# Performance work log

Hardware: AMD Instinct MI355X
Metric: run time of the kernel (lower is better)

Reference implementation:

```python
import jax, jax.numpy as jnp
import numpy as np

B = 65536          # number of graphs
NPG = 28           # nodes per graph (896 = 32*28)
N = B * NPG
K = 4              # random within-graph neighbors per node


def setup_inputs() -> dict:
    key = jax.random.key(0)
    ks = jax.random.split(key, 8)
    x = jax.random.normal(ks[0], (N, 2), dtype=jnp.float32)
    # within-graph random edges: each node i -> K random targets in its graph
    local = jax.random.randint(ks[1], (N, K), 0, NPG)
    base = (jnp.arange(N, dtype=jnp.int32) // NPG) * NPG
    dst = (base[:, None] + local.astype(jnp.int32)).reshape(-1)
    src = jnp.repeat(jnp.arange(N, dtype=jnp.int32), K)
    edge_index = jnp.stack([src, dst])  # [2, E]
    conv_w = jax.random.normal(ks[2], (2, 32), dtype=jnp.float32) * (1.0 / np.sqrt(2))
    conv_b = jax.random.normal(ks[3], (32,), dtype=jnp.float32) * 0.01
    fc1_w = jax.random.normal(ks[4], (896, 256), dtype=jnp.float32) * (1.0 / np.sqrt(896))
    fc1_b = jax.random.normal(ks[5], (256,), dtype=jnp.float32) * 0.01
    fc2_w = jax.random.normal(ks[6], (256, 2), dtype=jnp.float32) * (1.0 / np.sqrt(256))
    fc2_b = jax.random.normal(ks[7], (2,), dtype=jnp.float32) * 0.01
    return {"x": x, "edge_index": edge_index, "conv_w": conv_w, "conv_b": conv_b,
            "fc1_w": fc1_w, "fc1_b": fc1_b, "fc2_w": fc2_w, "fc2_b": fc2_b}


def gcn_conv(x, edge_index, w, b):
    n = x.shape[0]
    h = x @ w  # [N, 32]
    loops = jnp.arange(n, dtype=edge_index.dtype)
    src = jnp.concatenate([edge_index[0], loops])
    dst = jnp.concatenate([edge_index[1], loops])
    deg = jax.ops.segment_sum(jnp.ones_like(dst, dtype=h.dtype), dst, num_segments=n)
    dinv = jnp.where(deg > 0, jax.lax.rsqrt(jnp.maximum(deg, 1.0)), 0.0)
    norm = dinv[src] * dinv[dst]  # [E']
    agg = jax.ops.segment_sum(h[src] * norm[:, None], dst, num_segments=n)
    return agg + b


def reference(x, edge_index, conv_w, conv_b, fc1_w, fc1_b, fc2_w, fc2_b):
    h = jax.nn.relu(gcn_conv(x, edge_index, conv_w, conv_b))  # [N, 32]
    h = h.reshape(-1, 896)                                    # [B, 896]
    h = h @ fc1_w + fc1_b                                     # [B, 256]
    nrm = jnp.sqrt(jnp.sum(h * h, axis=1, keepdims=True))
    hn = h / jnp.maximum(nrm, 1e-12)                          # F.normalize(dim=1)
    x1 = hn @ fc2_w + fc2_b                                   # [B, 2]
    mu = jax.nn.sigmoid(x1[:, 0])
    theta = jax.nn.softplus(x1[:, 1])
    return hn, mu, theta
```

## Files before the change

kernel.cpp:

```cpp
#include <hip/hip_runtime.h>
#include <hip/hip_bf16.h>
#include <stdint.h>

#define NPG 28
#define KDIM 896
#define NOUT 256
#define BM 64
#define BK 32
#define KT (KDIM / BK)

typedef __attribute__((ext_vector_type(8))) __bf16 bf16x8;
typedef __attribute__((ext_vector_type(8))) ushort us8;
typedef __attribute__((ext_vector_type(4))) float f32x4;

__device__ __forceinline__ ushort f2bf(float v) {
    uint u = __float_as_uint(v);
    return (ushort)((u + 0x7fffu + ((u >> 16) & 1u)) >> 16);
}

__device__ __forceinline__ void gload_lds16(const void* g, void* l) {
    __builtin_amdgcn_global_load_lds(
        (const __attribute__((address_space(1))) void*)(uintptr_t)g,
        (__attribute__((address_space(3))) void*)(uintptr_t)l,
        16, 0, 0);
}

__global__ __launch_bounds__(256) void k_agg(
    const float* __restrict__ x, const int* __restrict__ dst,
    const float* __restrict__ f1w,
    float* __restrict__ acc2g, ushort* __restrict__ wt, int nAgg)
{
    __shared__ int   pk[8][32];
    __shared__ float sx[8][32][2];
    __shared__ float t[32][33];

    const int tid = threadIdx.x;

    if ((int)blockIdx.x >= nAgg) {
        int b = blockIdx.x - nAgg;
        int n0 = (b & 7) * 32, k0 = (b >> 3) * 32;
        int tx = tid & 31, ty = tid >> 5;
#pragma unroll
        for (int q = 0; q < 4; ++q)
            t[ty + q * 8][tx] = f1w[(k0 + ty + q * 8) * NOUT + n0 + tx];
        __syncthreads();
#pragma unroll
        for (int q = 0; q < 4; ++q)
            wt[(long)(n0 + ty + q * 8) * KDIM + k0 + tx] = f2bf(t[tx][ty + q * 8]);
        return;
    }

    const int g = tid >> 5;
    const int j = tid & 31;
    const long gb = ((long)blockIdx.x * 8 + g) * NPG;

    float2 xx = make_float2(0.f, 0.f);
    if (j < NPG) {
        int4 d4 = ((const int4*)dst)[gb + j];
        xx = ((const float2*)x)[gb + j];
        int gbi = (int)gb;
        pk[g][j] = (d4.x - gbi) | ((d4.y - gbi) << 8) |
                   ((d4.z - gbi) << 16) | ((d4.w - gbi) << 24);
    }
    __syncthreads();

    const uint repj = (uint)j * 0x01010101u;
    uint cp0 = 0, cp1 = 0, cp2 = 0, cp3 = 0;
    int cnt = 0;
#pragma unroll
    for (int s4 = 0; s4 < 7; ++s4) {
        int4 pv = *(const int4*)&pk[g][s4 * 4];
#pragma unroll
        for (int r = 0; r < 4; ++r) {
            uint v = ((const uint*)&pv)[r] ^ repj;
            uint zb = ~(((v & 0x7F7F7F7Fu) + 0x7F7F7F7Fu) | v) & 0x80808080u;
            uint c = (uint)__popc(zb);
            cnt += (int)c;
            int s = s4 * 4 + r;
            uint nib = c << ((s & 7) * 4);
            if (s < 8)       cp0 |= nib;
            else if (s < 16) cp1 |= nib;
            else if (s < 24) cp2 |= nib;
            else             cp3 |= nib;
        }
    }

    const float dinv = rsqrtf((float)(1 + cnt));
    const float sx0 = xx.x * dinv, sx1 = xx.y * dinv;
    if (j < NPG) {
        sx[g][j][0] = sx0;
        sx[g][j][1] = sx1;
    }
    __syncthreads();

    float a0 = sx0, a1 = sx1;
#pragma unroll
    for (int s = 0; s < NPG; ++s) {
        float2 sv = *(const float2*)&sx[g][s][0];
        uint cpw = (s < 8) ? cp0 : (s < 16) ? cp1 : (s < 24) ? cp2 : cp3;
        float cf = (float)((cpw >> ((s & 7) * 4)) & 0xFu);
        a0 += cf * sv.x;
        a1 += cf * sv.y;
    }

    if (j < NPG) {
        const long Btot = (long)nAgg * 8;
        const long graph = (long)blockIdx.x * 8 + g;
        ((float2*)acc2g)[(long)j * Btot + graph] = make_float2(a0 * dinv, a1 * dinv);
    }
}

__device__ __forceinline__ void stage_b4(const char* WtB, ushort* BsX, int kt, int w, int l) {
    const int o = (l & 3) ^ ((l >> 3) & 3);
#pragma unroll
    for (int i = 0; i < 4; ++i) {
        int row = w * 64 + i * 16 + (l >> 2);
        gload_lds16(WtB + (long)row * (KDIM * 2) + kt * 64 + o * 16,
                    (char*)BsX + w * 4096 + i * 1024);
    }
}

__device__ __forceinline__ void agen_write(ushort* AsX, float2 av, int awoff,
                                           const float* w0, const float* w1, const float* bb) {
    union { us8 v; uint u[4]; } pk;
#pragma unroll
    for (int k = 0; k < 4; ++k) {
        float e0 = fmaxf(av.x * w0[2 * k]     + av.y * w1[2 * k]     + bb[2 * k],     0.f);
        float e1 = fmaxf(av.x * w0[2 * k + 1] + av.y * w1[2 * k + 1] + bb[2 * k + 1], 0.f);
        __hip_bfloat162 h = __float22bfloat162_rn(make_float2(e0, e1));
        pk.u[k] = *reinterpret_cast<uint*>(&h);
    }
    *(us8*)&AsX[awoff] = pk.v;
}

__device__ __forceinline__ void compute_mfma(const ushort* AsX, const ushort* BsX,
                                             f32x4 acc[4][4], int a_off, int b_off) {
    bf16x8 bfr[4], afr[4];
#pragma unroll
    for (int ni = 0; ni < 4; ++ni)
        bfr[ni] = *(const bf16x8*)(&BsX[b_off + ni * 512]);
#pragma unroll
    for (int mi = 0; mi < 4; ++mi)
        afr[mi] = *(const bf16x8*)(&AsX[a_off + mi * 512]);
    __builtin_amdgcn_s_setprio(1);
#pragma unroll
    for (int mi = 0; mi < 4; ++mi)
#pragma unroll
        for (int ni = 0; ni < 4; ++ni)
            acc[mi][ni] = __builtin_amdgcn_mfma_f32_16x16x32_bf16(
                afr[mi], bfr[ni], acc[mi][ni], 0, 0, 0);
    __builtin_amdgcn_s_setprio(0);
}

__global__ __launch_bounds__(256, 3) void k_gemm(
    const float* __restrict__ acc2g, const ushort* __restrict__ Wt,
    const float* __restrict__ cw, const float* __restrict__ cb,
    const float* __restrict__ f1b, const float* __restrict__ f2w,
    const float* __restrict__ f2b, float* __restrict__ out, int Bsz)
{
    __shared__ ushort As0[BM * BK], As1[BM * BK];
    __shared__ ushort Bs0[NOUT * BK], Bs1[NOUT * BK];

    const int tid = threadIdx.x;
    const int w = tid >> 6, l = tid & 63;
    const int l15 = l & 15, lhi = (l >> 4) & 3;
    const long m0 = (long)blockIdx.x * BM;
    const long Btot = Bsz;

    const int ao = __builtin_amdgcn_readfirstlane(w);
    const int awoff = l * 32 + ((ao ^ ((l >> 1) & 3)) * 8);
    float w0[8], w1[8], bb[8];
#pragma unroll
    for (int k = 0; k < 8; ++k) {
        w0[k] = cw[ao * 8 + k]; w1[k] = cw[32 + ao * 8 + k]; bb[k] = cb[ao * 8 + k];
    }

    const int swz = (lhi ^ ((l15 >> 1) & 3)) * 8;
    const int a_off = l15 * 32 + swz;
    const int b_off = (w * 64 + l15) * 32 + swz;

    const float2* a2 = (const float2*)acc2g;
    const char* WtB = (const char*)Wt;
    const long ag = m0 + l;

    f32x4 acc[4][4];
#pragma unroll
    for (int mi = 0; mi < 4; ++mi)
#pragma unroll
        for (int ni = 0; ni < 4; ++ni) acc[mi][ni] = (f32x4){0.f, 0.f, 0.f, 0.f};

    {
        float2 av0 = a2[ag];
        stage_b4(WtB, Bs0, 0, w, l);
        agen_write(As0, av0, awoff, w0, w1, bb);
    }
    float2 avn = a2[Btot + ag];
    __syncthreads();

    for (int kt = 0; kt < KT - 2; kt += 2) {
        stage_b4(WtB, Bs1, kt + 1, w, l);
        float2 avn2 = a2[(long)(kt + 2) * Btot + ag];
        agen_write(As1, avn, awoff, w0, w1, bb);
        compute_mfma(As0, Bs0, acc, a_off, b_off);
        asm volatile("s_waitcnt lgkmcnt(0)" ::: "memory");
        __builtin_amdgcn_s_barrier();
        asm volatile("s_waitcnt vmcnt(0)" ::: "memory");

        stage_b4(WtB, Bs0, kt + 2, w, l);
        avn = a2[(long)(kt + 3) * Btot + ag];
        agen_write(As0, avn2, awoff, w0, w1, bb);
        compute_mfma(As1, Bs1, acc, a_off, b_off);
        asm volatile("s_waitcnt lgkmcnt(0)" ::: "memory");
        __builtin_amdgcn_s_barrier();
        asm volatile("s_waitcnt vmcnt(0)" ::: "memory");
    }
    {
        stage_b4(WtB, Bs1, KT - 1, w, l);
        agen_write(As1, avn, awoff, w0, w1, bb);
        compute_mfma(As0, Bs0, acc, a_off, b_off);
        asm volatile("s_waitcnt lgkmcnt(0)" ::: "memory");
        __builtin_amdgcn_s_barrier();
        asm volatile("s_waitcnt vmcnt(0)" ::: "memory");
        compute_mfma(As1, Bs1, acc, a_off, b_off);
    }
    __syncthreads();

    float b1[4], w20[4], w21[4];
#pragma unroll
    for (int ni = 0; ni < 4; ++ni) {
        int col = w * 64 + ni * 16 + l15;
        b1[ni] = f1b[col];
        w20[ni] = f2w[col * 2 + 0];
        w21[ni] = f2w[col * 2 + 1];
    }
    float* red    = (float*)As0;
    float* red_ss = red;
    float* red_p0 = red + 256;
    float* red_p1 = red + 512;
    float* red_rn = red + 768;

#pragma unroll
    for (int mi = 0; mi < 4; ++mi) {
        float ssr[4], p0r[4], p1r[4];
#pragma unroll
        for (int r = 0; r < 4; ++r) { ssr[r] = 0.f; p0r[r] = 0.f; p1r[r] = 0.f; }
#pragma unroll
        for (int ni = 0; ni < 4; ++ni) {
#pragma unroll
            for (int r = 0; r < 4; ++r) {
                float v = acc[mi][ni][r] + b1[ni];
                acc[mi][ni][r] = v;
                ssr[r] += v * v;
                p0r[r] += v * w20[ni];
                p1r[r] += v * w21[ni];
            }
        }
#pragma unroll
        for (int m = 1; m < 16; m <<= 1) {
#pragma unroll
            for (int r = 0; r < 4; ++r) {
                ssr[r] += __shfl_xor(ssr[r], m);
                p0r[r] += __shfl_xor(p0r[r], m);
                p1r[r] += __shfl_xor(p1r[r], m);
            }
        }
        if (l15 == 0) {
            int rowb = mi * 16 + lhi * 4;
#pragma unroll
            for (int r = 0; r < 4; ++r) {
                red_ss[(rowb + r) * 4 + w] = ssr[r];
                red_p0[(rowb + r) * 4 + w] = p0r[r];
                red_p1[(rowb + r) * 4 + w] = p1r[r];
            }
        }
    }
    __syncthreads();

    if (tid < BM) {
        int row = tid;
        float ss = red_ss[row * 4 + 0] + red_ss[row * 4 + 1] + red_ss[row * 4 + 2] + red_ss[row * 4 + 3];
        float p0 = red_p0[row * 4 + 0] + red_p0[row * 4 + 1] + red_p0[row * 4 + 2] + red_p0[row * 4 + 3];
        float p1 = red_p1[row * 4 + 0] + red_p1[row * 4 + 1] + red_p1[row * 4 + 2] + red_p1[row * 4 + 3];
        float rn = 1.0f / fmaxf(sqrtf(ss), 1e-12f);
        float x0 = p0 * rn + f2b[0];
        float x1 = p1 * rn + f2b[1];
        float mu = 1.0f / (1.0f + expf(-x0));
        float th = (x1 > 0.f) ? (x1 + log1pf(expf(-x1))) : log1pf(expf(x1));
        long gr = m0 + row;
        out[(long)Bsz * NOUT + gr] = mu;
        out[(long)Bsz * NOUT + Bsz + gr] = th;
        red_rn[row] = rn;
    }
    __syncthreads();

#pragma unroll
    for (int mi = 0; mi < 4; ++mi) {
        float rn[4];
#pragma unroll
        for (int r = 0; r < 4; ++r) rn[r] = red_rn[mi * 16 + lhi * 4 + r];
#pragma unroll
        for (int ni = 0; ni < 4; ++ni) {
#pragma unroll
            for (int r = 0; r < 4; ++r) {
                long row = m0 + mi * 16 + lhi * 4 + r;
                out[row * NOUT + w * 64 + ni * 16 + l15] = acc[mi][ni][r] * rn[r];
            }
        }
    }
}

extern "C" void kernel_launch(void* const* d_in, const int* in_sizes, int n_in,
                              void* d_out, int out_size, void* d_ws, size_t ws_size,
                              hipStream_t stream) {
    const float* x   = (const float*)d_in[0];
    const int*   ei  = (const int*)d_in[1];
    const float* cw  = (const float*)d_in[2];
    const float* cb  = (const float*)d_in[3];
    const float* f1w = (const float*)d_in[4];
    const float* f1b = (const float*)d_in[5];
    const float* f2w = (const float*)d_in[6];
    const float* f2b = (const float*)d_in[7];
    float* out = (float*)d_out;

    const int Nn  = in_sizes[0] / 2;
    const int Bsz = Nn / NPG;
    const int E   = in_sizes[1] / 2;
    const int* dst = ei + E;

    float*  acc2g = (float*)d_ws;
    ushort* Wt    = (ushort*)(acc2g + (size_t)Nn * 2);

    const int nAgg = Bsz / 8;
    const int nTr  = (KDIM / 32) * (NOUT / 32);

    k_agg<<<nAgg + nTr, 256, 0, stream>>>(x, dst, f1w, acc2g, Wt, nAgg);
    k_gemm<<<Bsz / BM, 256, 0, stream>>>(acc2g, Wt, cw, cb, f1b, f2w, f2b, out, Bsz);
}
```

Baseline: 78.30 us.

## Double GEMM M-tile to 128 rows and store fc1 weights k-tile-contiguous

Raises the GEMM block tile from 64 to 128 graphs, so each block runs 8x4 MFMA tiles per wave and reuses every staged B tile over twice as many rows. This halves the total fc1 weight traffic through LDS. The transpose kernel now writes bf16 weights in a k-tile-major layout, so each stage load reads one contiguous 16KB chunk. The cost is a doubled accumulator register footprint, with launch bounds cut from 3 to 2 blocks per CU, which lowers occupancy and latency hiding.

```diff
diff --git a/kernel.cpp b/kernel.cpp
--- a/kernel.cpp
+++ b/kernel.cpp
@@ -5,7 +5,7 @@
 #define NPG 28
 #define KDIM 896
 #define NOUT 256
-#define BM 64
+#define BM 128
 #define BK 32
 #define KT (KDIM / BK)
 
@@ -46,7 +46,8 @@
         __syncthreads();
 #pragma unroll
         for (int q = 0; q < 4; ++q)
-            wt[(long)(n0 + ty + q * 8) * KDIM + k0 + tx] = f2bf(t[tx][ty + q * 8]);
+            wt[(long)(k0 >> 5) * (NOUT * BK) + (n0 + ty + q * 8) * BK + tx] =
+                f2bf(t[tx][ty + q * 8]);
         return;
     }
 
@@ -115,7 +116,7 @@
 #pragma unroll
     for (int i = 0; i < 4; ++i) {
         int row = w * 64 + i * 16 + (l >> 2);
-        gload_lds16(WtB + (long)row * (KDIM * 2) + kt * 64 + o * 16,
+        gload_lds16(WtB + (long)kt * 16384 + row * 64 + o * 16,
                     (char*)BsX + w * 4096 + i * 1024);
     }
 }
@@ -134,25 +135,24 @@
 }
 
 __device__ __forceinline__ void compute_mfma(const ushort* AsX, const ushort* BsX,
-                                             f32x4 acc[4][4], int a_off, int b_off) {
-    bf16x8 bfr[4], afr[4];
+                                             f32x4 acc[8][4], int a_off, int b_off) {
+    bf16x8 bfr[4];
 #pragma unroll
     for (int ni = 0; ni < 4; ++ni)
         bfr[ni] = *(const bf16x8*)(&BsX[b_off + ni * 512]);
-#pragma unroll
-    for (int mi = 0; mi < 4; ++mi)
-        afr[mi] = *(const bf16x8*)(&AsX[a_off + mi * 512]);
     __builtin_amdgcn_s_setprio(1);
 #pragma unroll
-    for (int mi = 0; mi < 4; ++mi)
+    for (int mi = 0; mi < 8; ++mi) {
+        bf16x8 af = *(const bf16x8*)(&AsX[a_off + mi * 512]);
 #pragma unroll
         for (int ni = 0; ni < 4; ++ni)
             acc[mi][ni] = __builtin_amdgcn_mfma_f32_16x16x32_bf16(
-                afr[mi], bfr[ni], acc[mi][ni], 0, 0, 0);
+                af, bfr[ni], acc[mi][ni], 0, 0, 0);
+    }
     __builtin_amdgcn_s_setprio(0);
 }
 
-__global__ __launch_bounds__(256, 3) void k_gemm(
+__global__ __launch_bounds__(256, 2) void k_gemm(
     const float* __restrict__ acc2g, const ushort* __restrict__ Wt,
     const float* __restrict__ cw, const float* __restrict__ cb,
     const float* __restrict__ f1b, const float* __restrict__ f2w,
@@ -168,7 +168,9 @@
     const long Btot = Bsz;
 
     const int ao = __builtin_amdgcn_readfirstlane(w);
-    const int awoff = l * 32 + ((ao ^ ((l >> 1) & 3)) * 8);
+    const int axor = (ao ^ ((l >> 1) & 3)) * 8;
+    const int awoff_lo = l * 32 + axor;
+    const int awoff_hi = (l + 64) * 32 + axor;
     float w0[8], w1[8], bb[8];
 #pragma unroll
     for (int k = 0; k < 8; ++k) {
@@ -183,32 +185,38 @@
     const char* WtB = (const char*)Wt;
     const long ag = m0 + l;
 
-    f32x4 acc[4][4];
-#pragma unroll
-    for (int mi = 0; mi < 4; ++mi)
+    f32x4 acc[8][4];
+#pragma unroll
+    for (int mi = 0; mi < 8; ++mi)
 #pragma unroll
         for (int ni = 0; ni < 4; ++ni) acc[mi][ni] = (f32x4){0.f, 0.f, 0.f, 0.f};
 
     {
-        float2 av0 = a2[ag];
+        float2 alo = a2[ag];
+        float2 ahi = a2[ag + 64];
         stage_b4(WtB, Bs0, 0, w, l);
-        agen_write(As0, av0, awoff, w0, w1, bb);
-    }
-    float2 avn = a2[Btot + ag];
+        agen_write(As0, alo, awoff_lo, w0, w1, bb);
+        agen_write(As0, ahi, awoff_hi, w0, w1, bb);
+    }
+    float2 nlo = a2[Btot + ag], nhi = a2[Btot + ag + 64];
     __syncthreads();
 
     for (int kt = 0; kt < KT - 2; kt += 2) {
         stage_b4(WtB, Bs1, kt + 1, w, l);
-        float2 avn2 = a2[(long)(kt + 2) * Btot + ag];
-        agen_write(As1, avn, awoff, w0, w1, bb);
+        float2 n2lo = a2[(long)(kt + 2) * Btot + ag];
+        float2 n2hi = a2[(long)(kt + 2) * Btot + ag + 64];
+        agen_write(As1, nlo, awoff_lo, w0, w1, bb);
+        agen_write(As1, nhi, awoff_hi, w0, w1, bb);
         compute_mfma(As0, Bs0, acc, a_off, b_off);
         asm volatile("s_waitcnt lgkmcnt(0)" ::: "memory");
         __builtin_amdgcn_s_barrier();
         asm volatile("s_waitcnt vmcnt(0)" ::: "memory");
 
         stage_b4(WtB, Bs0, kt + 2, w, l);
-        avn = a2[(long)(kt + 3) * Btot + ag];
-        agen_write(As0, avn2, awoff, w0, w1, bb);
+        nlo = a2[(long)(kt + 3) * Btot + ag];
+        nhi = a2[(long)(kt + 3) * Btot + ag + 64];
+        agen_write(As0, n2lo, awoff_lo, w0, w1, bb);
+        agen_write(As0, n2hi, awoff_hi, w0, w1, bb);
         compute_mfma(As1, Bs1, acc, a_off, b_off);
         asm volatile("s_waitcnt lgkmcnt(0)" ::: "memory");
         __builtin_amdgcn_s_barrier();
@@ -216,7 +224,8 @@
     }
     {
         stage_b4(WtB, Bs1, KT - 1, w, l);
-        agen_write(As1, avn, awoff, w0, w1, bb);
+        agen_write(As1, nlo, awoff_lo, w0, w1, bb);
+        agen_write(As1, nhi, awoff_hi, w0, w1, bb);
         compute_mfma(As0, Bs0, acc, a_off, b_off);
         asm volatile("s_waitcnt lgkmcnt(0)" ::: "memory");
         __builtin_amdgcn_s_barrier();
@@ -233,14 +242,14 @@
         w20[ni] = f2w[col * 2 + 0];
         w21[ni] = f2w[col * 2 + 1];
     }
-    float* red    = (float*)As0;
+    float* red    = (float*)Bs0;
     float* red_ss = red;
-    float* red_p0 = red + 256;
-    float* red_p1 = red + 512;
-    float* red_rn = red + 768;
-
-#pragma unroll
-    for (int mi = 0; mi < 4; ++mi) {
+    float* red_p0 = red + 512;
+    float* red_p1 = red + 1024;
+    float* red_rn = red + 1536;
+
+#pragma unroll
+    for (int mi = 0; mi < 8; ++mi) {
         float ssr[4], p0r[4], p1r[4];
 #pragma unroll
         for (int r = 0; r < 4; ++r) { ssr[r] = 0.f; p0r[r] = 0.f; p1r[r] = 0.f; }
@@ -294,7 +303,7 @@
     __syncthreads();
 
 #pragma unroll
-    for (int mi = 0; mi < 4; ++mi) {
+    for (int mi = 0; mi < 8; ++mi) {
         float rn[4];
 #pragma unroll
         for (int r = 0; r < 4; ++r) rn[r] = red_rn[mi * 16 + lhi * 4 + r];
```

After: 67.69 us. -13.6%, faster.
